# Kernel tuning notes

Hardware: AMD Instinct MI355X
Metric: run time of the kernel (lower is better)

Reference implementation:

```python
import jax, jax.numpy as jnp
import numpy as np

LO = 30            # rollout horizon (hard-coded in SimCore)
AS_DIM = 400       # ssbm_actionstate_dim
HEAD = AS_DIM + 7  # per-player decoder width


def setup_inputs() -> dict:
    key = jax.random.key(0)
    ks = jax.random.split(key, 12)
    T, B, A, H = 128, 256, 64, 1024
    Nt, Ng = 6, 4
    Lu = T - 1 - LO
    s = 0.02
    return dict(
        observations=jax.random.uniform(ks[0], (T, B, 16), jnp.float32),
        actions=jax.random.normal(ks[1], (T, B, A), jnp.float32),
        beliefs=jax.random.normal(ks[2], (T, B, H), jnp.float32),
        w_ih=jax.random.normal(ks[3], (3 * H, A), jnp.float32) * s,
        w_hh=jax.random.normal(ks[4], (3 * H, H), jnp.float32) * s,
        b_ih=jnp.zeros((3 * H,), jnp.float32),
        b_hh=jnp.zeros((3 * H,), jnp.float32),
        pre_w1=jax.random.normal(ks[5], (64, H), jnp.float32) * s,
        pre_b1=jnp.zeros((64,), jnp.float32),
        pre_w2=jax.random.normal(ks[6], (H, 64), jnp.float32) * s,
        pre_b2=jnp.zeros((H,), jnp.float32),
        dec_w=jax.random.normal(ks[7], (2 * HEAD, H), jnp.float32) * s,
        dec_b=jnp.zeros((2 * HEAD,), jnp.float32),
        idx_i=jax.random.randint(ks[8], (Nt,), 0, Lu, dtype=jnp.int32),
        K=jax.random.randint(ks[9], (Nt, Ng), 0, LO, dtype=jnp.int32),
    )


def _bce_logits(x, t):
    # binary_cross_entropy_with_logits, elementwise
    return jax.nn.softplus(x) - x * t


def _player_loss(pred, tgt):
    # pred: [Nt,Ng,B,407] logits; tgt: [Nt,Ng,B,8] observation half
    # pytorch means are over everything except the Nt python loop -> mean over (Ng,B[,feat])
    logits = pred[..., :AS_DIM]
    cls = tgt[..., 0].astype(jnp.int32)                     # .long() of float target
    ce = -jnp.take_along_axis(jax.nn.log_softmax(logits, -1), cls[..., None], -1)[..., 0]
    loss = ce.mean(axis=(1, 2))
    loss = loss + ((pred[..., 400:402] - tgt[..., 1:3]) ** 2).mean(axis=(1, 2, 3))
    loss = loss + ((jax.nn.softplus(pred[..., 402:403]) - tgt[..., 3:4]) ** 2).mean(axis=(1, 2, 3))
    loss = loss + ((jax.nn.softplus(pred[..., 403:404]) - tgt[..., 4:5]) ** 2).mean(axis=(1, 2, 3))
    loss = loss + _bce_logits(pred[..., 404:405], tgt[..., 5:6]).mean(axis=(1, 2, 3))
    loss = loss + _bce_logits(pred[..., 405:406], tgt[..., 6:7]).mean(axis=(1, 2, 3))
    loss = loss + _bce_logits(pred[..., 406:407], tgt[..., 7:8]).mean(axis=(1, 2, 3))
    return loss  # [Nt]


def reference(observations, actions, beliefs, w_ih, w_hh, b_ih, b_hh,
              pre_w1, pre_b1, pre_w2, pre_b2, dec_w, dec_b, idx_i, K):
    def gru_cell(h, a):
        gi = a @ w_ih.T + b_ih              # [B,3H]
        gh = h @ w_hh.T + b_hh
        ir, iz, in_ = jnp.split(gi, 3, axis=-1)
        hr, hz, hn = jnp.split(gh, 3, axis=-1)
        r = jax.nn.sigmoid(ir + hr)
        z = jax.nn.sigmoid(iz + hz)
        n = jnp.tanh(in_ + r * hn)
        h_new = (1.0 - z) * n + z * h
        return h_new, h_new

    def rollout(i, k):
        h0 = beliefs[i]                                          # [B,H]
        acts = jax.lax.dynamic_slice_in_dim(actions, i, LO, axis=0)
        _, states = jax.lax.scan(gru_cell, h0, acts)             # [Lo,B,H]
        return states[k], observations[k + i + 1]                # [Ng,B,H],[Ng,B,16]

    states, obs = jax.vmap(rollout)(idx_i, K)                    # [Nt,Ng,B,H]

    # ResidualBlock: x + relu(relu(x W1^T + b1) W2^T + b2)
    h = jax.nn.relu(states @ pre_w1.T + pre_b1)
    x = states + jax.nn.relu(h @ pre_w2.T + pre_b2)

    logits = x @ dec_w.T + dec_b                                 # [Nt,Ng,B,814]
    agent, opponent = logits[..., :HEAD], logits[..., HEAD:]
    tgt_a, tgt_o = obs[..., :8], obs[..., 8:]

    loss = (_player_loss(agent, tgt_a) + _player_loss(opponent, tgt_o)).sum()
    return loss
```

## Files before the change

kernel.cpp:

```cpp
#include <hip/hip_runtime.h>
#include <hip/hip_bf16.h>

typedef __bf16 bf16;
typedef __attribute__((ext_vector_type(4))) __bf16 bf16x4;
typedef __attribute__((ext_vector_type(8))) __bf16 bf16x8;
typedef __attribute__((ext_vector_type(4))) float f32x4;

static __device__ __forceinline__ f32x4 MFMA(bf16x8 a, bf16x8 b, f32x4 c) {
  return __builtin_amdgcn_mfma_f32_16x16x32_bf16(a, b, c, 0, 0, 0);
}

__device__ __forceinline__ float sigm(float x) { return 1.0f / (1.0f + __expf(-x)); }
__device__ __forceinline__ float softplus_(float x) {
  return fmaxf(x, 0.0f) + log1pf(__expf(-fabsf(x)));
}

__device__ __forceinline__ void gl16(const bf16* g, char* l) {
  __builtin_amdgcn_global_load_lds(
      (const __attribute__((address_space(1))) char*)g,
      (__attribute__((address_space(3))) char*)l, 16, 0, 0);
}

__global__ void k_prep(const float* __restrict__ whh, const float* __restrict__ wih,
                       const float* __restrict__ act, const float* __restrict__ w1,
                       const float* __restrict__ w2, const float* __restrict__ dw,
                       const float* __restrict__ beliefs, const int* __restrict__ idx_i,
                       bf16* __restrict__ Whd, bf16* __restrict__ Wid,
                       bf16* __restrict__ actd, bf16* __restrict__ w1d,
                       bf16* __restrict__ w2d, bf16* __restrict__ dwd,
                       bf16* __restrict__ hAd) {
  for (int q = blockIdx.x * blockDim.x + threadIdx.x; q < 1994240;
       q += gridDim.x * blockDim.x) {
    const float* src;
    bf16* dst;
    int off;
    if (q < 786432)       { src = whh; dst = Whd;  off = q; }
    else if (q < 835584)  { src = wih; dst = Wid;  off = q - 786432; }
    else if (q < 1359872) { src = act; dst = actd; off = q - 835584; }
    else if (q < 1376256) { src = w1;  dst = w1d;  off = q - 1359872; }
    else if (q < 1392640) { src = w2;  dst = w2d;  off = q - 1376256; }
    else if (q < 1601024) { src = dw;  dst = dwd;  off = q - 1392640; }
    else {
      const int e = (q - 1601024) << 2;
      const int n = e >> 18, rest = e & 262143;
      float4 v = *(const float4*)&beliefs[((size_t)idx_i[n] << 18) + rest];
      bf16x4 o = {(bf16)v.x, (bf16)v.y, (bf16)v.z, (bf16)v.w};
      *(bf16x4*)&hAd[e] = o;
      continue;
    }
    float4 v = *(const float4*)&src[(size_t)off << 2];
    bf16x4 o = {(bf16)v.x, (bf16)v.y, (bf16)v.z, (bf16)v.w};
    *(bf16x4*)&dst[(size_t)off << 2] = o;
  }
}

__global__ __launch_bounds__(256, 2) void k_gru_step(
    const bf16* __restrict__ hin, bf16* __restrict__ hout,
    const bf16* __restrict__ Wh, const bf16* __restrict__ Wi,
    const bf16* __restrict__ actB,
    const float* __restrict__ b_ih, const float* __restrict__ b_hh,
    const int* __restrict__ idx_i, const int* __restrict__ Kmat,
    bf16* __restrict__ states, int step) {
  const int pid = blockIdx.x;
  const int xcd = pid & 7;
  const int rg = xcd >> 2;
  const int cgp = xcd & 3;
  const int q = pid >> 3;
  const int mtl = q & 7;
  const int jtl = q >> 3;
  const int m0 = rg * 768 + mtl * 96;
  const int j0 = (cgp * 8 + jtl) * 32;

  const int tid = threadIdx.x, wave = tid >> 6, lane = tid & 63;
  const int l15 = lane & 15;
  const int kgrp = lane >> 4;
  const int wm = wave >> 1;
  const int wj = wave & 1;
  const int jlane = j0 + wj * 16 + l15;

  __shared__ alignas(16) bf16 As[3][96][64];
  __shared__ alignas(16) bf16 Bs[3][96][64];

  const int srow = lane >> 3;
  const int scol = (((lane & 7) ^ srow) << 3);

  const bf16* asrc[3];
  const bf16* bsrc[3];
  const bf16* aisrc[3];
  const bf16* bisrc[3];
#pragma unroll
  for (int i = 0; i < 3; ++i) {
    const int prow = wave * 24 + i * 8 + srow;
    const int grow = m0 + prow;
    asrc[i] = hin + (size_t)grow * 1024 + scol;
    const int wr = (prow >> 5) * 1024 + j0 + (prow & 31);
    bsrc[i] = Wh + (size_t)wr * 1024 + scol;
    bisrc[i] = Wi + (size_t)wr * 64 + scol;
    const int np = grow >> 8;
    aisrc[i] = actB + ((size_t)(idx_i[np] + step) * 256 + (grow & 255)) * 64 + scol;
  }

  auto stage = [&](int buf, int it) {
    char* ad = (char*)As + buf * 12288 + (wave * 24) * 128;
    char* bd = (char*)Bs + buf * 12288 + (wave * 24) * 128;
    if (it < 16) {
#pragma unroll
      for (int i = 0; i < 3; ++i) {
        gl16(asrc[i] + it * 64, ad + i * 1024);
        gl16(bsrc[i] + it * 64, bd + i * 1024);
      }
    } else {
#pragma unroll
      for (int i = 0; i < 3; ++i) {
        gl16(aisrc[i], ad + i * 1024);
        gl16(bisrc[i], bd + i * 1024);
      }
    }
  };

  f32x4 accR[3], accZ[3], accNh[3], accNi[3];
  const f32x4 zero = {0.f, 0.f, 0.f, 0.f};
#pragma unroll
  for (int f = 0; f < 3; ++f) { accR[f] = zero; accZ[f] = zero; accNh[f] = zero; accNi[f] = zero; }

  const float br = b_ih[jlane] + b_hh[jlane];
  const float bz = b_ih[1024 + jlane] + b_hh[1024 + jlane];
  const float bin = b_ih[2048 + jlane];
  const float bhn = b_hh[2048 + jlane];

  auto compute = [&](int buf, f32x4 (&gN)[3]) {
    const char* ab = (const char*)As + buf * 12288;
    const char* bb = (const char*)Bs + buf * 12288;
#pragma unroll
    for (int kkI = 0; kkI < 2; ++kkI) {
      const int kbyte = (((kkI << 5) + (kgrp << 3)) << 1) ^ ((l15 & 7) << 4);
      bf16x8 a0 = *(const bf16x8*)(ab + (wm * 48 + l15) * 128 + kbyte);
      bf16x8 a1 = *(const bf16x8*)(ab + (wm * 48 + 16 + l15) * 128 + kbyte);
      bf16x8 a2 = *(const bf16x8*)(ab + (wm * 48 + 32 + l15) * 128 + kbyte);
      bf16x8 b_r = *(const bf16x8*)(bb + (wj * 16 + l15) * 128 + kbyte);
      bf16x8 b_z = *(const bf16x8*)(bb + (32 + wj * 16 + l15) * 128 + kbyte);
      bf16x8 b_n = *(const bf16x8*)(bb + (64 + wj * 16 + l15) * 128 + kbyte);
      accR[0] = MFMA(a0, b_r, accR[0]);
      accR[1] = MFMA(a1, b_r, accR[1]);
      accR[2] = MFMA(a2, b_r, accR[2]);
      accZ[0] = MFMA(a0, b_z, accZ[0]);
      accZ[1] = MFMA(a1, b_z, accZ[1]);
      accZ[2] = MFMA(a2, b_z, accZ[2]);
      gN[0] = MFMA(a0, b_n, gN[0]);
      gN[1] = MFMA(a1, b_n, gN[1]);
      gN[2] = MFMA(a2, b_n, gN[2]);
    }
  };

  stage(0, 0);
  stage(1, 1);

#pragma unroll
  for (int t = 0; t < 17; ++t) {
    if (t < 15) stage((t + 2) % 3, t + 2);
    if (t < 15)       asm volatile("s_waitcnt vmcnt(12)" ::: "memory");
    else if (t == 15) asm volatile("s_waitcnt vmcnt(6)" ::: "memory");
    else              asm volatile("s_waitcnt vmcnt(0)" ::: "memory");
    __builtin_amdgcn_s_barrier();
    if (t == 16) compute(16 % 3, accNi);
    else         compute(t % 3, accNh);
    __builtin_amdgcn_sched_barrier(0);
    __builtin_amdgcn_s_barrier();
  }

#pragma unroll
  for (int mf = 0; mf < 3; ++mf) {
    const int mbase = m0 + wm * 48 + mf * 16 + kgrp * 4;
    const int n = mbase >> 8;
    const int k0 = Kmat[n * 4 + 0], k1 = Kmat[n * 4 + 1];
    const int k2 = Kmat[n * 4 + 2], k3 = Kmat[n * 4 + 3];
#pragma unroll
    for (int ii = 0; ii < 4; ++ii) {
      const int m = mbase + ii;
      float rg2 = sigm(accR[mf][ii] + br);
      float zg = sigm(accZ[mf][ii] + bz);
      float ng = tanhf(accNi[mf][ii] + bin + rg2 * (accNh[mf][ii] + bhn));
      float hp = (float)hin[(size_t)m * 1024 + jlane];
      float hnew = (1.0f - zg) * ng + zg * hp;
      bf16 hb = (bf16)hnew;
      hout[(size_t)m * 1024 + jlane] = hb;
      const int b = m & 255;
      if (k0 == step) states[((size_t)(n * 4 + 0) * 256 + b) * 1024 + jlane] = hb;
      if (k1 == step) states[((size_t)(n * 4 + 1) * 256 + b) * 1024 + jlane] = hb;
      if (k2 == step) states[((size_t)(n * 4 + 2) * 256 + b) * 1024 + jlane] = hb;
      if (k3 == step) states[((size_t)(n * 4 + 3) * 256 + b) * 1024 + jlane] = hb;
    }
  }
}

template <int EPI, int SWZ>
__global__ __launch_bounds__(256) void k_gemm_epi(
    const bf16* __restrict__ A, const bf16* __restrict__ W, int K, int Nreal, int ld_out,
    const float* __restrict__ bias, const bf16* __restrict__ resid,
    float* __restrict__ outF, bf16* __restrict__ outB) {
  int mt, jt;
  if (SWZ) {
    const int lin = blockIdx.x;
    const int x = lin & 7, k = lin >> 3;
    mt = 12 * x + k % 12;
    jt = k / 12;
  } else {
    mt = blockIdx.x;
    jt = blockIdx.y;
  }
  const int m0 = mt * 64;
  const int j0 = jt * 64;
  const int tid = threadIdx.x, wave = tid >> 6, lane = tid & 63;
  __shared__ alignas(16) bf16 Al[64][72];
  __shared__ alignas(16) bf16 Wl[64][72];

  f32x4 acc[4];
  const f32x4 zero = {0.f, 0.f, 0.f, 0.f};
#pragma unroll
  for (int f = 0; f < 4; ++f) acc[f] = zero;

  const int r = tid >> 3, c8 = (tid & 7) << 3;
  const int arow = wave * 16 + (lane & 15);
  const int koff = (lane >> 4) << 3;

  for (int kb = 0; kb < K; kb += 64) {
    *(bf16x8*)&Al[r][c8]      = *(const bf16x8*)&A[(size_t)(m0 + r) * K + kb + c8];
    *(bf16x8*)&Al[r + 32][c8] = *(const bf16x8*)&A[(size_t)(m0 + r + 32) * K + kb + c8];
    int jr = j0 + r;      if (jr >= Nreal) jr = Nreal - 1;
    int jr2 = j0 + r + 32; if (jr2 >= Nreal) jr2 = Nreal - 1;
    *(bf16x8*)&Wl[r][c8]      = *(const bf16x8*)&W[(size_t)jr * K + kb + c8];
    *(bf16x8*)&Wl[r + 32][c8] = *(const bf16x8*)&W[(size_t)jr2 * K + kb + c8];
    __syncthreads();
#pragma unroll
    for (int kk = 0; kk < 64; kk += 32) {
      bf16x8 av = *(const bf16x8*)&Al[arow][kk + koff];
#pragma unroll
      for (int nf = 0; nf < 4; ++nf) {
        acc[nf] = MFMA(av, *(const bf16x8*)&Wl[nf * 16 + (lane & 15)][kk + koff], acc[nf]);
      }
    }
    __syncthreads();
  }

#pragma unroll
  for (int nf = 0; nf < 4; ++nf) {
    int j = j0 + nf * 16 + (lane & 15);
    float bj = (j < Nreal) ? bias[j] : 0.f;
#pragma unroll
    for (int i = 0; i < 4; ++i) {
      int m = m0 + wave * 16 + ((lane >> 4) << 2) + i;
      float v = acc[nf][i] + bj;
      if (EPI == 0) {
        outB[(size_t)m * ld_out + j] = (bf16)fmaxf(v, 0.f);
      } else if (EPI == 1) {
        v = fmaxf(v, 0.f) + (float)resid[(size_t)m * ld_out + j];
        outB[(size_t)m * ld_out + j] = (bf16)v;
      } else {
        if (j < Nreal) outF[(size_t)m * ld_out + j] = v;
      }
    }
  }
}

__global__ __launch_bounds__(256) void k_loss_rows(
    const float* __restrict__ logits, const float* __restrict__ obs,
    const int* __restrict__ idx_i, const int* __restrict__ Kmat,
    float* __restrict__ partials) {
  const int row = blockIdx.x;
  const int n = row >> 10, g = (row >> 8) & 3, b = row & 255;
  const int i = idx_i[n], k = Kmat[n * 4 + g];
  const float* L = logits + (size_t)row * 814;
  const float* ob = obs + ((size_t)(k + i + 1) * 256 + b) * 16;
  const int tid = threadIdx.x, lane = tid & 63, wv = tid >> 6;
  __shared__ float red[4];

  float total = 0.f;
#pragma unroll
  for (int p = 0; p < 2; ++p) {
    const float* Lp = L + p * 407;
    const float* tg = ob + p * 8;
    float mx = -1e30f;
    for (int c = tid; c < 400; c += 256) mx = fmaxf(mx, Lp[c]);
#pragma unroll
    for (int s = 32; s; s >>= 1) mx = fmaxf(mx, __shfl_xor(mx, s));
    __syncthreads();
    if (lane == 0) red[wv] = mx;
    __syncthreads();
    mx = fmaxf(fmaxf(red[0], red[1]), fmaxf(red[2], red[3]));
    __syncthreads();
    float se = 0.f;
    for (int c = tid; c < 400; c += 256) se += __expf(Lp[c] - mx);
#pragma unroll
    for (int s = 32; s; s >>= 1) se += __shfl_xor(se, s);
    if (lane == 0) red[wv] = se;
    __syncthreads();
    se = red[0] + red[1] + red[2] + red[3];
    __syncthreads();

    if (tid == 0) {
      int cls = (int)tg[0];
      float lse = mx + logf(se);
      float v = lse - Lp[cls];
      float d0 = Lp[400] - tg[1], d1 = Lp[401] - tg[2];
      v += 0.5f * (d0 * d0 + d1 * d1);
      float s2 = softplus_(Lp[402]) - tg[3]; v += s2 * s2;
      float s3 = softplus_(Lp[403]) - tg[4]; v += s3 * s3;
      v += softplus_(Lp[404]) - Lp[404] * tg[5];
      v += softplus_(Lp[405]) - Lp[405] * tg[6];
      v += softplus_(Lp[406]) - Lp[406] * tg[7];
      total += v;
    }
    __syncthreads();
  }
  if (tid == 0) partials[row] = total * (1.0f / 1024.0f);
}

__global__ void k_reduce_final(const float* __restrict__ partials, float* __restrict__ out) {
  __shared__ float s[256];
  float v = 0.f;
  for (int i = threadIdx.x; i < 6144; i += 256) v += partials[i];
  s[threadIdx.x] = v;
  __syncthreads();
  for (int st = 128; st; st >>= 1) {
    if (threadIdx.x < st) s[threadIdx.x] += s[threadIdx.x + st];
    __syncthreads();
  }
  if (threadIdx.x == 0) out[0] = s[0];
}


extern "C" void kernel_launch(void* const* d_in, const int* in_sizes, int n_in,
                              void* d_out, int out_size, void* d_ws, size_t ws_size,
                              hipStream_t stream) {
  const float* obs      = (const float*)d_in[0];
  const float* actions  = (const float*)d_in[1];
  const float* beliefs  = (const float*)d_in[2];
  const float* w_ih     = (const float*)d_in[3];
  const float* w_hh     = (const float*)d_in[4];
  const float* b_ih     = (const float*)d_in[5];
  const float* b_hh     = (const float*)d_in[6];
  const float* pre_w1   = (const float*)d_in[7];
  const float* pre_b1   = (const float*)d_in[8];
  const float* pre_w2   = (const float*)d_in[9];
  const float* pre_b2   = (const float*)d_in[10];
  const float* dec_w    = (const float*)d_in[11];
  const float* dec_b    = (const float*)d_in[12];
  const int*   idx_i    = (const int*)d_in[13];
  const int*   Kmat     = (const int*)d_in[14];
  float* outF = (float*)d_out;

  char* p = (char*)d_ws;
  auto carve = [&](size_t bytes) {
    char* q = p;
    p += (bytes + 255) & ~(size_t)255;
    return q;
  };
  bf16* Wh      = (bf16*)carve(3072u * 1024u * 2u);
  bf16* Wi      = (bf16*)carve(3072u * 64u * 2u);
  bf16* actBv   = (bf16*)carve(128u * 256u * 64u * 2u);
  bf16* preW1b  = (bf16*)carve(64u * 1024u * 2u);
  bf16* preW2b  = (bf16*)carve(1024u * 64u * 2u);
  bf16* decWb   = (bf16*)carve(814u * 1024u * 2u);
  bf16* hA      = (bf16*)carve(1536u * 1024u * 2u);
  bf16* hB      = (bf16*)carve(1536u * 1024u * 2u);
  bf16* states  = (bf16*)carve(6144u * 1024u * 2u);
  bf16* h1      = (bf16*)carve(6144u * 64u * 2u);
  bf16* xbuf    = (bf16*)carve(6144u * 1024u * 2u);
  float* logits = (float*)carve((size_t)6144u * 814u * 4u);
  float* partials = (float*)carve(6144u * 4u);

  k_prep<<<2048, 256, 0, stream>>>(w_hh, w_ih, actions, pre_w1, pre_w2, dec_w,
                                   beliefs, idx_i, Wh, Wi, actBv, preW1b, preW2b,
                                   decWb, hA);

  for (int t = 0; t < 30; ++t) {
    const bf16* hi = (t & 1) ? hB : hA;
    bf16* ho = (t & 1) ? hA : hB;
    k_gru_step<<<512, 256, 0, stream>>>(hi, ho, Wh, Wi, actBv, b_ih, b_hh,
                                        idx_i, Kmat, states, t);
  }

  k_gemm_epi<0, 0><<<dim3(96, 1), 256, 0, stream>>>(states, preW1b, 1024, 64, 64,
                                                    pre_b1, nullptr, nullptr, h1);
  k_gemm_epi<1, 1><<<1536, 256, 0, stream>>>(h1, preW2b, 64, 1024, 1024,
                                             pre_b2, states, nullptr, xbuf);
  k_gemm_epi<2, 1><<<1248, 256, 0, stream>>>(xbuf, decWb, 1024, 814, 814,
                                             dec_b, nullptr, logits, nullptr);

  k_loss_rows<<<6144, 256, 0, stream>>>(logits, obs, idx_i, Kmat, partials);
  k_reduce_final<<<1, 256, 0, stream>>>(partials, outF);
}
```

Measured before the change: 662.4 us.

## Load GRU hidden-state operand directly into registers and use three waves per block

The GRU step kernel no longer stages the hidden-state (A) tile through LDS. Each wave now loads its own 32 rows of A straight from global memory into registers, in a three-slot register ring that follows the LDS ring for weights. Only the weight tile still goes through LDS, and the block shrinks from four to three waves, each covering 32 rows by the full 32-column gate tile. This removes the LDS traffic and space for A, at the cost of more registers and less latency hiding from fewer waves.

After: 788.5 us. +19.0%, slower.

```diff
diff --git a/kernel.cpp b/kernel.cpp
--- a/kernel.cpp
+++ b/kernel.cpp
@@ -54,7 +54,7 @@
   }
 }
 
-__global__ __launch_bounds__(256, 2) void k_gru_step(
+__global__ __launch_bounds__(192, 2) void k_gru_step(
     const bf16* __restrict__ hin, bf16* __restrict__ hout,
     const bf16* __restrict__ Wh, const bf16* __restrict__ Wi,
     const bf16* __restrict__ actB,
@@ -71,124 +71,145 @@
   const int m0 = rg * 768 + mtl * 96;
   const int j0 = (cgp * 8 + jtl) * 32;
 
-  const int tid = threadIdx.x, wave = tid >> 6, lane = tid & 63;
+  const int tid = threadIdx.x;
+  const int wave = tid / 64, lane = tid & 63;
   const int l15 = lane & 15;
   const int kgrp = lane >> 4;
-  const int wm = wave >> 1;
-  const int wj = wave & 1;
-  const int jlane = j0 + wj * 16 + l15;
-
-  __shared__ alignas(16) bf16 As[3][96][64];
+
   __shared__ alignas(16) bf16 Bs[3][96][64];
 
   const int srow = lane >> 3;
   const int scol = (((lane & 7) ^ srow) << 3);
 
-  const bf16* asrc[3];
-  const bf16* bsrc[3];
-  const bf16* aisrc[3];
-  const bf16* bisrc[3];
-#pragma unroll
-  for (int i = 0; i < 3; ++i) {
-    const int prow = wave * 24 + i * 8 + srow;
-    const int grow = m0 + prow;
-    asrc[i] = hin + (size_t)grow * 1024 + scol;
+  const bf16* wsrc[4];
+  const bf16* wisrc[4];
+#pragma unroll
+  for (int i = 0; i < 4; ++i) {
+    const int prow = wave * 32 + i * 8 + srow;
     const int wr = (prow >> 5) * 1024 + j0 + (prow & 31);
-    bsrc[i] = Wh + (size_t)wr * 1024 + scol;
-    bisrc[i] = Wi + (size_t)wr * 64 + scol;
-    const int np = grow >> 8;
-    aisrc[i] = actB + ((size_t)(idx_i[np] + step) * 256 + (grow & 255)) * 64 + scol;
-  }
+    wsrc[i] = Wh + (size_t)wr * 1024 + scol;
+    wisrc[i] = Wi + (size_t)wr * 64 + scol;
+  }
+
+  const int arow0 = m0 + wave * 32 + l15;
+  const bf16* aB0 = hin + (size_t)arow0 * 1024 + kgrp * 8;
+  const bf16* aB1 = aB0 + (size_t)16 * 1024;
+  const int nA0 = arow0 >> 8, nA1 = (arow0 + 16) >> 8;
+  const bf16* actA0 =
+      actB + ((size_t)(idx_i[nA0] + step) * 256 + (arow0 & 255)) * 64 + kgrp * 8;
+  const bf16* actA1 =
+      actB + ((size_t)(idx_i[nA1] + step) * 256 + ((arow0 + 16) & 255)) * 64 + kgrp * 8;
 
   auto stage = [&](int buf, int it) {
-    char* ad = (char*)As + buf * 12288 + (wave * 24) * 128;
-    char* bd = (char*)Bs + buf * 12288 + (wave * 24) * 128;
+    char* dst = (char*)Bs + buf * 12288 + (wave * 32) * 128;
     if (it < 16) {
 #pragma unroll
-      for (int i = 0; i < 3; ++i) {
-        gl16(asrc[i] + it * 64, ad + i * 1024);
-        gl16(bsrc[i] + it * 64, bd + i * 1024);
-      }
+      for (int i = 0; i < 4; ++i) gl16(wsrc[i] + it * 64, dst + i * 1024);
     } else {
 #pragma unroll
-      for (int i = 0; i < 3; ++i) {
-        gl16(aisrc[i], ad + i * 1024);
-        gl16(bisrc[i], bd + i * 1024);
-      }
+      for (int i = 0; i < 4; ++i) gl16(wisrc[i], dst + i * 1024);
     }
   };
 
-  f32x4 accR[3], accZ[3], accNh[3], accNi[3];
+  bf16x8 areg[3][4];
+  auto loadA = [&](int bank, int it) {
+    if (it < 16) {
+      areg[bank][0] = *(const bf16x8*)(aB0 + it * 64);
+      areg[bank][1] = *(const bf16x8*)(aB0 + it * 64 + 32);
+      areg[bank][2] = *(const bf16x8*)(aB1 + it * 64);
+      areg[bank][3] = *(const bf16x8*)(aB1 + it * 64 + 32);
+    } else {
+      areg[bank][0] = *(const bf16x8*)(actA0);
+      areg[bank][1] = *(const bf16x8*)(actA0 + 32);
+      areg[bank][2] = *(const bf16x8*)(actA1);
+      areg[bank][3] = *(const bf16x8*)(actA1 + 32);
+    }
+  };
+
+  f32x4 accR[2][2], accZ[2][2], accNh[2][2], accNi[2][2];
   const f32x4 zero = {0.f, 0.f, 0.f, 0.f};
 #pragma unroll
-  for (int f = 0; f < 3; ++f) { accR[f] = zero; accZ[f] = zero; accNh[f] = zero; accNi[f] = zero; }
-
-  const float br = b_ih[jlane] + b_hh[jlane];
-  const float bz = b_ih[1024 + jlane] + b_hh[1024 + jlane];
-  const float bin = b_ih[2048 + jlane];
-  const float bhn = b_hh[2048 + jlane];
-
-  auto compute = [&](int buf, f32x4 (&gN)[3]) {
-    const char* ab = (const char*)As + buf * 12288;
-    const char* bb = (const char*)Bs + buf * 12288;
+  for (int a = 0; a < 2; ++a)
+#pragma unroll
+    for (int b = 0; b < 2; ++b) {
+      accR[a][b] = zero; accZ[a][b] = zero; accNh[a][b] = zero; accNi[a][b] = zero;
+    }
+
+  float brc[2], bzc[2], binc[2], bhnc[2];
+#pragma unroll
+  for (int jh = 0; jh < 2; ++jh) {
+    const int j = j0 + jh * 16 + l15;
+    brc[jh] = b_ih[j] + b_hh[j];
+    bzc[jh] = b_ih[1024 + j] + b_hh[1024 + j];
+    binc[jh] = b_ih[2048 + j];
+    bhnc[jh] = b_hh[2048 + j];
+  }
+
+  auto compute = [&](int slot, f32x4 (&gN)[2][2]) {
+    const char* bb = (const char*)Bs + slot * 12288;
 #pragma unroll
     for (int kkI = 0; kkI < 2; ++kkI) {
       const int kbyte = (((kkI << 5) + (kgrp << 3)) << 1) ^ ((l15 & 7) << 4);
-      bf16x8 a0 = *(const bf16x8*)(ab + (wm * 48 + l15) * 128 + kbyte);
-      bf16x8 a1 = *(const bf16x8*)(ab + (wm * 48 + 16 + l15) * 128 + kbyte);
-      bf16x8 a2 = *(const bf16x8*)(ab + (wm * 48 + 32 + l15) * 128 + kbyte);
-      bf16x8 b_r = *(const bf16x8*)(bb + (wj * 16 + l15) * 128 + kbyte);
-      bf16x8 b_z = *(const bf16x8*)(bb + (32 + wj * 16 + l15) * 128 + kbyte);
-      bf16x8 b_n = *(const bf16x8*)(bb + (64 + wj * 16 + l15) * 128 + kbyte);
-      accR[0] = MFMA(a0, b_r, accR[0]);
-      accR[1] = MFMA(a1, b_r, accR[1]);
-      accR[2] = MFMA(a2, b_r, accR[2]);
-      accZ[0] = MFMA(a0, b_z, accZ[0]);
-      accZ[1] = MFMA(a1, b_z, accZ[1]);
-      accZ[2] = MFMA(a2, b_z, accZ[2]);
-      gN[0] = MFMA(a0, b_n, gN[0]);
-      gN[1] = MFMA(a1, b_n, gN[1]);
-      gN[2] = MFMA(a2, b_n, gN[2]);
+      bf16x8 br0 = *(const bf16x8*)(bb + (l15) * 128 + kbyte);
+      bf16x8 br1 = *(const bf16x8*)(bb + (16 + l15) * 128 + kbyte);
+      bf16x8 bz0 = *(const bf16x8*)(bb + (32 + l15) * 128 + kbyte);
+      bf16x8 bz1 = *(const bf16x8*)(bb + (48 + l15) * 128 + kbyte);
+      bf16x8 bn0 = *(const bf16x8*)(bb + (64 + l15) * 128 + kbyte);
+      bf16x8 bn1 = *(const bf16x8*)(bb + (80 + l15) * 128 + kbyte);
+#pragma unroll
+      for (int mf = 0; mf < 2; ++mf) {
+        bf16x8 a = areg[slot][mf * 2 + kkI];
+        accR[mf][0] = MFMA(a, br0, accR[mf][0]);
+        accR[mf][1] = MFMA(a, br1, accR[mf][1]);
+        accZ[mf][0] = MFMA(a, bz0, accZ[mf][0]);
+        accZ[mf][1] = MFMA(a, bz1, accZ[mf][1]);
+        gN[mf][0] = MFMA(a, bn0, gN[mf][0]);
+        gN[mf][1] = MFMA(a, bn1, gN[mf][1]);
+      }
     }
   };
 
-  stage(0, 0);
-  stage(1, 1);
+  stage(0, 0); loadA(0, 0);
+  stage(1, 1); loadA(1, 1);
 
 #pragma unroll
   for (int t = 0; t < 17; ++t) {
-    if (t < 15) stage((t + 2) % 3, t + 2);
-    if (t < 15)       asm volatile("s_waitcnt vmcnt(12)" ::: "memory");
-    else if (t == 15) asm volatile("s_waitcnt vmcnt(6)" ::: "memory");
+    if (t < 15) { stage((t + 2) % 3, t + 2); loadA((t + 2) % 3, t + 2); }
+    if (t <= 14)      asm volatile("s_waitcnt vmcnt(16)" ::: "memory");
+    else if (t == 15) asm volatile("s_waitcnt vmcnt(8)" ::: "memory");
     else              asm volatile("s_waitcnt vmcnt(0)" ::: "memory");
     __builtin_amdgcn_s_barrier();
-    if (t == 16) compute(16 % 3, accNi);
+    if (t == 16) compute(1, accNi);
     else         compute(t % 3, accNh);
     __builtin_amdgcn_sched_barrier(0);
     __builtin_amdgcn_s_barrier();
   }
 
 #pragma unroll
-  for (int mf = 0; mf < 3; ++mf) {
-    const int mbase = m0 + wm * 48 + mf * 16 + kgrp * 4;
+  for (int mf = 0; mf < 2; ++mf) {
+    const int mbase = m0 + wave * 32 + mf * 16 + kgrp * 4;
     const int n = mbase >> 8;
     const int k0 = Kmat[n * 4 + 0], k1 = Kmat[n * 4 + 1];
     const int k2 = Kmat[n * 4 + 2], k3 = Kmat[n * 4 + 3];
 #pragma unroll
-    for (int ii = 0; ii < 4; ++ii) {
-      const int m = mbase + ii;
-      float rg2 = sigm(accR[mf][ii] + br);
-      float zg = sigm(accZ[mf][ii] + bz);
-      float ng = tanhf(accNi[mf][ii] + bin + rg2 * (accNh[mf][ii] + bhn));
-      float hp = (float)hin[(size_t)m * 1024 + jlane];
-      float hnew = (1.0f - zg) * ng + zg * hp;
-      bf16 hb = (bf16)hnew;
-      hout[(size_t)m * 1024 + jlane] = hb;
-      const int b = m & 255;
-      if (k0 == step) states[((size_t)(n * 4 + 0) * 256 + b) * 1024 + jlane] = hb;
-      if (k1 == step) states[((size_t)(n * 4 + 1) * 256 + b) * 1024 + jlane] = hb;
-      if (k2 == step) states[((size_t)(n * 4 + 2) * 256 + b) * 1024 + jlane] = hb;
-      if (k3 == step) states[((size_t)(n * 4 + 3) * 256 + b) * 1024 + jlane] = hb;
+    for (int jh = 0; jh < 2; ++jh) {
+      const int j = j0 + jh * 16 + l15;
+#pragma unroll
+      for (int ii = 0; ii < 4; ++ii) {
+        const int m = mbase + ii;
+        float rgt = sigm(accR[mf][jh][ii] + brc[jh]);
+        float zg = sigm(accZ[mf][jh][ii] + bzc[jh]);
+        float ng = tanhf(accNi[mf][jh][ii] + binc[jh] + rgt * (accNh[mf][jh][ii] + bhnc[jh]));
+        float hp = (float)hin[(size_t)m * 1024 + j];
+        float hnew = (1.0f - zg) * ng + zg * hp;
+        bf16 hb = (bf16)hnew;
+        hout[(size_t)m * 1024 + j] = hb;
+        const int b = m & 255;
+        if (k0 == step) states[((size_t)(n * 4 + 0) * 256 + b) * 1024 + j] = hb;
+        if (k1 == step) states[((size_t)(n * 4 + 1) * 256 + b) * 1024 + j] = hb;
+        if (k2 == step) states[((size_t)(n * 4 + 2) * 256 + b) * 1024 + j] = hb;
+        if (k3 == step) states[((size_t)(n * 4 + 3) * 256 + b) * 1024 + j] = hb;
+      }
     }
   }
 }
@@ -376,7 +397,7 @@
   for (int t = 0; t < 30; ++t) {
     const bf16* hi = (t & 1) ? hB : hA;
     bf16* ho = (t & 1) ? hA : hB;
-    k_gru_step<<<512, 256, 0, stream>>>(hi, ho, Wh, Wi, actBv, b_ih, b_hh,
+    k_gru_step<<<512, 192, 0, stream>>>(hi, ho, Wh, Wi, actBv, b_ih, b_hh,
                                         idx_i, Kmat, states, t);
   }
 
```
